# Performance work log

Hardware: AMD Instinct MI355X
Metric: run time of the kernel (lower is better)

## Reference

```python
import jax, jax.numpy as jnp
import numpy as np

R = 32  # voxel resolution


def setup_inputs() -> dict:
    key = jax.random.key(0)
    k1, k2 = jax.random.split(key)
    B, C, N = 8, 64, 100000
    features = jax.random.normal(k1, (B, C, N), dtype=jnp.float32)
    coords = jax.random.uniform(k2, (B, 3, N), dtype=jnp.float32)  # unit cube [0,1]
    return {"features": features, "coords": coords}


def reference(features, coords):
    # features: [B, C, N], coords: [B, 3, N] in [0, 1]
    B, C, N = features.shape
    norm_coords = jnp.clip(coords * R, 0, R - 1)
    vox_coords = jnp.round(norm_coords).astype(jnp.int32)  # [B, 3, N]

    # flat voxel index per point: x*R^2 + y*R + z, offset per batch
    idx = vox_coords[:, 0] * R * R + vox_coords[:, 1] * R + vox_coords[:, 2]  # [B, N]
    flat_idx = (idx + jnp.arange(B, dtype=jnp.int32)[:, None] * (R ** 3)).reshape(-1)  # [B*N]

    feat = jnp.transpose(features, (0, 2, 1)).reshape(B * N, C)  # [B*N, C]
    sums = jax.ops.segment_sum(feat, flat_idx, num_segments=B * R ** 3)  # [B*R^3, C]
    cnt = jax.ops.segment_sum(jnp.ones((B * N,), features.dtype), flat_idx,
                              num_segments=B * R ** 3)  # [B*R^3]
    avg = sums / jnp.maximum(cnt, 1.0)[:, None]  # average; empty voxels stay 0

    vox_feat = jnp.transpose(avg.reshape(B, R ** 3, C), (0, 2, 1)).reshape(B, C, R, R, R)
    return vox_feat, vox_coords.astype(jnp.int64)
```

## Files before the change

### kernel.cpp

```cpp
#include <hip/hip_runtime.h>

#define RR 32
#define R3 32768
#define BATCH 8
#define CH 64
#define NPTS 100000
#define NPOINTS (BATCH * NPTS)
#define NVOX (BATCH * R3)
#define SCAN_BLOCKS (NVOX / 256)
#define HBLK 32
#define PPB (NPTS / HBLK)

typedef unsigned int uint32;

__device__ __forceinline__ uint32 f2bf(float f) {
    uint32 u = __float_as_uint(f);
    return (u + 0x7fffu + ((u >> 16) & 1u)) >> 16;
}
__device__ __forceinline__ float bf2f(uint32 h) {
    return __uint_as_float(h << 16);
}

__global__ __launch_bounds__(256) void voxhist(
    const float* __restrict__ coords,
    uint32* __restrict__ vox,
    uint32* __restrict__ phist,
    float* __restrict__ out2)
{
    __shared__ uint32 hist[R3];

    int b   = blockIdx.x >> 5;
    int blk = blockIdx.x & 31;
    int tid = threadIdx.x;

    for (int i = tid; i < R3; i += 256) hist[i] = 0u;
    __syncthreads();

    int n0 = blk * PPB;
    const float* cb = coords + (size_t)b * 3 * NPTS;
    float*       o2 = out2   + (size_t)b * 3 * NPTS;

    for (int i = tid; i < PPB; i += 256) {
        int n = n0 + i;
        float fx = fminf(fmaxf(cb[n]            * 32.0f, 0.0f), 31.0f);
        float fy = fminf(fmaxf(cb[NPTS + n]     * 32.0f, 0.0f), 31.0f);
        float fz = fminf(fmaxf(cb[2 * NPTS + n] * 32.0f, 0.0f), 31.0f);
        int x = (int)rintf(fx);
        int y = (int)rintf(fy);
        int z = (int)rintf(fz);
        int v = x * (RR * RR) + y * RR + z;

        o2[n]            = (float)x;
        o2[NPTS + n]     = (float)y;
        o2[2 * NPTS + n] = (float)z;

        vox[(size_t)b * NPTS + n] = (uint32)(b * R3 + v);
        atomicAdd(&hist[v], 1u);
    }
    __syncthreads();

    uint32* ph = phist + (size_t)(b * HBLK + blk) * R3;
    for (int i = tid; i < R3; i += 256) ph[i] = hist[i];
}

__global__ __launch_bounds__(256) void scan_hist_sums(
    const uint32* __restrict__ phist,
    uint32* __restrict__ cnt, uint32* __restrict__ bsum)
{
    __shared__ uint32 s[256];
    int t = threadIdx.x;
    int gid = blockIdx.x * 256 + t;
    int b = gid >> 15;
    int v = gid & (R3 - 1);

    const uint32* ph = phist + (size_t)b * HBLK * R3 + v;
    uint32 c = 0;
#pragma unroll
    for (int k = 0; k < HBLK; ++k) c += ph[(size_t)k * R3];
    cnt[gid] = c;

    s[t] = c;
    __syncthreads();
    for (int off = 128; off > 0; off >>= 1) {
        if (t < off) s[t] += s[t + off];
        __syncthreads();
    }
    if (t == 0) bsum[blockIdx.x] = s[0];
}

__global__ __launch_bounds__(256) void scan_bsum(uint32* __restrict__ bsum)
{
    __shared__ uint32 s[256];
    int t = threadIdx.x;
    uint32 v0 = bsum[4 * t], v1 = bsum[4 * t + 1], v2 = bsum[4 * t + 2], v3 = bsum[4 * t + 3];
    uint32 tot = v0 + v1 + v2 + v3;
    s[t] = tot;
    __syncthreads();
    for (int off = 1; off < 256; off <<= 1) {
        uint32 x = (t >= off) ? s[t - off] : 0u;
        __syncthreads();
        s[t] += x;
        __syncthreads();
    }
    uint32 excl = s[t] - tot;
    bsum[4 * t]     = excl;
    bsum[4 * t + 1] = excl + v0;
    bsum[4 * t + 2] = excl + v0 + v1;
    bsum[4 * t + 3] = excl + v0 + v1 + v2;
}

__global__ __launch_bounds__(256) void scan_final(
    const uint32* __restrict__ cnt, const uint32* __restrict__ bsum,
    uint32* __restrict__ starts, uint32* __restrict__ cursor)
{
    __shared__ uint32 s[256];
    int t = threadIdx.x;
    int gid = blockIdx.x * 256 + t;
    uint32 v = cnt[gid];
    s[t] = v;
    __syncthreads();
    for (int off = 1; off < 256; off <<= 1) {
        uint32 x = (t >= off) ? s[t - off] : 0u;
        __syncthreads();
        s[t] += x;
        __syncthreads();
    }
    uint32 st = bsum[blockIdx.x] + s[t] - v;
    starts[gid] = st;
    cursor[gid] = st;
}

__global__ __launch_bounds__(256) void phase3_scatter(
    const float* __restrict__ feat,
    const uint32* __restrict__ vox,
    uint32* __restrict__ cursor,
    uint4* __restrict__ sorted)
{
    int gid = blockIdx.x * blockDim.x + threadIdx.x;
    if (gid >= NPOINTS) return;
    int b = gid / NPTS;
    int n = gid - b * NPTS;

    uint32 g = vox[gid];
    uint32 pos = atomicAdd(&cursor[g], 1u);

    const float* frow = feat + (size_t)b * CH * NPTS + n;
    uint4* dst = sorted + (size_t)pos * 8;
#pragma unroll
    for (int j = 0; j < 8; ++j) {
        uint4 w;
        float f0 = frow[(size_t)(8 * j + 0) * NPTS];
        float f1 = frow[(size_t)(8 * j + 1) * NPTS];
        float f2 = frow[(size_t)(8 * j + 2) * NPTS];
        float f3 = frow[(size_t)(8 * j + 3) * NPTS];
        float f4 = frow[(size_t)(8 * j + 4) * NPTS];
        float f5 = frow[(size_t)(8 * j + 5) * NPTS];
        float f6 = frow[(size_t)(8 * j + 6) * NPTS];
        float f7 = frow[(size_t)(8 * j + 7) * NPTS];
        w.x = f2bf(f0) | (f2bf(f1) << 16);
        w.y = f2bf(f2) | (f2bf(f3) << 16);
        w.z = f2bf(f4) | (f2bf(f5) << 16);
        w.w = f2bf(f6) | (f2bf(f7) << 16);
        dst[j] = w;
    }
}

__global__ __launch_bounds__(256) void phase4_reduce(
    const uint32* __restrict__ sorted,
    const uint32* __restrict__ starts,
    float* __restrict__ out1)
{
    __shared__ float tile[64][65];

    int gbase = blockIdx.x * 64;
    int tid = threadIdx.x;
    int w = tid >> 6, lane = tid & 63;
    int half = lane >> 5;
    int cp   = lane & 31;

    for (int k = 0; k < 16; ++k) {
        int g = gbase + w * 16 + k;
        uint32 s = starts[g];
        uint32 e = (g == NVOX - 1) ? (uint32)NPOINTS : starts[g + 1];
        float a0 = 0.0f, a1 = 0.0f;
        for (uint32 p = s + half; p < e; p += 2) {
            uint32 d = sorted[(size_t)p * 32 + cp];
            a0 += bf2f(d & 0xffffu);
            a1 += bf2f(d >> 16);
        }
        a0 += __shfl_xor(a0, 32);
        a1 += __shfl_xor(a1, 32);
        if (half == 0) {
            uint32 c = e - s;
            float rcp = 1.0f / (float)(c > 1u ? c : 1u);
            int vloc = w * 16 + k;
            tile[vloc][2 * cp]     = a0 * rcp;
            tile[vloc][2 * cp + 1] = a1 * rcp;
        }
    }
    __syncthreads();

    int b = gbase / R3;
    int v0 = gbase - b * R3;
    int vv = tid & 63;
    int c0 = tid >> 6;
    float* obase = out1 + (size_t)b * CH * R3 + v0 + vv;
#pragma unroll
    for (int jj = 0; jj < 16; ++jj) {
        int c = jj * 4 + c0;
        obase[(size_t)c * R3] = tile[vv][c];
    }
}

__global__ __launch_bounds__(256) void accum_direct(
    const float* __restrict__ feat, const float* __restrict__ coords,
    float* __restrict__ out1, uint32* __restrict__ cnt, float* __restrict__ out2)
{
    int gid = blockIdx.x * blockDim.x + threadIdx.x;
    if (gid >= NPOINTS) return;
    int b = gid / NPTS;
    int n = gid - b * NPTS;
    const float* cb = coords + (size_t)b * 3 * NPTS + n;
    float fx = fminf(fmaxf(cb[0]        * 32.0f, 0.0f), 31.0f);
    float fy = fminf(fmaxf(cb[NPTS]     * 32.0f, 0.0f), 31.0f);
    float fz = fminf(fmaxf(cb[2 * NPTS] * 32.0f, 0.0f), 31.0f);
    int x = (int)rintf(fx), y = (int)rintf(fy), z = (int)rintf(fz);
    int v = x * (RR * RR) + y * RR + z;
    float* o2 = out2 + (size_t)b * 3 * NPTS + n;
    o2[0] = (float)x; o2[NPTS] = (float)y; o2[2 * NPTS] = (float)z;
    atomicAdd(&cnt[b * R3 + v], 1u);
    float* obase = out1 + (size_t)(b * CH) * R3 + v;
    const float* frow = feat + (size_t)(b * CH) * NPTS + n;
#pragma unroll 8
    for (int c = 0; c < CH; ++c)
        unsafeAtomicAdd(&obase[(size_t)c * R3], frow[(size_t)c * NPTS]);
}

__global__ __launch_bounds__(256) void finalize_direct(
    float* __restrict__ out1, const uint32* __restrict__ cnt)
{
    size_t gid = (size_t)blockIdx.x * blockDim.x + threadIdx.x;
    size_t total = (size_t)BATCH * CH * R3;
    if (gid >= total) return;
    int v = (int)(gid & (R3 - 1));
    int b = (int)(gid / ((size_t)CH * R3));
    uint32 ct = cnt[b * R3 + v];
    out1[gid] = out1[gid] / (float)(ct > 1u ? ct : 1u);
}

extern "C" void kernel_launch(void* const* d_in, const int* in_sizes, int n_in,
                              void* d_out, int out_size, void* d_ws, size_t ws_size,
                              hipStream_t stream)
{
    const float* feat   = (const float*)d_in[0];
    const float* coords = (const float*)d_in[1];

    float* out1 = (float*)d_out;
    float* out2 = out1 + (size_t)BATCH * CH * R3;

    const size_t vox_off    = 0;
    const size_t vox_bytes  = (size_t)NPOINTS * 4;
    const size_t cnt_off    = vox_off + ((vox_bytes + 255) & ~255ull);
    const size_t cnt_bytes  = (size_t)NVOX * 4;
    const size_t starts_off = cnt_off + ((cnt_bytes + 255) & ~255ull);
    const size_t cursor_off = starts_off + ((cnt_bytes + 255) & ~255ull);
    const size_t bsum_off   = cursor_off + ((cnt_bytes + 255) & ~255ull);
    const size_t bsum_bytes = (size_t)SCAN_BLOCKS * 4;
    const size_t sort_off   = (bsum_off + bsum_bytes + 255) & ~255ull;
    const size_t sort_bytes = (size_t)NPOINTS * 128;
    const size_t need       = sort_off + sort_bytes;

    const int npt_blocks = (NPOINTS + 255) / 256;

    if (ws_size >= need) {
        char* ws = (char*)d_ws;
        uint32* vox    = (uint32*)(ws + vox_off);
        uint32* cnt    = (uint32*)(ws + cnt_off);
        uint32* starts = (uint32*)(ws + starts_off);
        uint32* cursor = (uint32*)(ws + cursor_off);
        uint32* bsum   = (uint32*)(ws + bsum_off);
        uint32* sorted = (uint32*)(ws + sort_off);
        uint32* phist  = sorted;

        voxhist<<<BATCH * HBLK, 256, 0, stream>>>(coords, vox, phist, out2);
        scan_hist_sums<<<SCAN_BLOCKS, 256, 0, stream>>>(phist, cnt, bsum);
        scan_bsum<<<1, 256, 0, stream>>>(bsum);
        scan_final<<<SCAN_BLOCKS, 256, 0, stream>>>(cnt, bsum, starts, cursor);
        phase3_scatter<<<npt_blocks, 256, 0, stream>>>(feat, vox, cursor, (uint4*)sorted);
        phase4_reduce<<<NVOX / 64, 256, 0, stream>>>(sorted, starts, out1);
    } else {
        uint32* cnt = (uint32*)d_ws;
        hipMemsetAsync(out1, 0, (size_t)BATCH * CH * R3 * sizeof(float), stream);
        hipMemsetAsync(d_ws, 0, (size_t)NVOX * 4, stream);
        accum_direct<<<npt_blocks, 256, 0, stream>>>(feat, coords, out1, cnt, out2);
        size_t total = (size_t)BATCH * CH * R3;
        finalize_direct<<<(unsigned)((total + 255) / 256), 256, 0, stream>>>(out1, cnt);
    }
}
```

Before: 445.0 us.

## Split scatter into coalesced bf16 transpose plus index-only counting sort and gather-reduce

Replaces the per-point scatter, which read 64 strided feature values and wrote a 128-byte bf16 row to a sorted position, with a shared-memory tiled transpose that writes point-major bf16 features coalesced. The scatter kernel now writes only a 4-byte point index, and the reduce kernel gathers feature rows through that index. Voxel indices are also stored as 16-bit values, and histogram clear and copy use 16-byte vector accesses. The aim is to replace strided, uncoalesced feature reads with coalesced ones, at the cost of an extra indirection and random row gathers in the reduce.

```diff
diff --git a/kernel.cpp b/kernel.cpp
--- a/kernel.cpp
+++ b/kernel.cpp
@@ -10,8 +10,10 @@
 #define SCAN_BLOCKS (NVOX / 256)
 #define HBLK 32
 #define PPB (NPTS / HBLK)
+#define NTILE 1563
 
 typedef unsigned int uint32;
+typedef unsigned short uint16;
 
 __device__ __forceinline__ uint32 f2bf(float f) {
     uint32 u = __float_as_uint(f);
@@ -23,7 +25,7 @@
 
 __global__ __launch_bounds__(256) void voxhist(
     const float* __restrict__ coords,
-    uint32* __restrict__ vox,
+    uint16* __restrict__ vox,
     uint32* __restrict__ phist,
     float* __restrict__ out2)
 {
@@ -33,7 +35,8 @@
     int blk = blockIdx.x & 31;
     int tid = threadIdx.x;
 
-    for (int i = tid; i < R3; i += 256) hist[i] = 0u;
+    uint4 z4 = make_uint4(0u, 0u, 0u, 0u);
+    for (int i = tid; i < R3 / 4; i += 256) ((uint4*)hist)[i] = z4;
     __syncthreads();
 
     int n0 = blk * PPB;
@@ -54,13 +57,13 @@
         o2[NPTS + n]     = (float)y;
         o2[2 * NPTS + n] = (float)z;
 
-        vox[(size_t)b * NPTS + n] = (uint32)(b * R3 + v);
+        vox[(size_t)b * NPTS + n] = (uint16)v;
         atomicAdd(&hist[v], 1u);
     }
     __syncthreads();
 
-    uint32* ph = phist + (size_t)(b * HBLK + blk) * R3;
-    for (int i = tid; i < R3; i += 256) ph[i] = hist[i];
+    uint4* ph = (uint4*)(phist + (size_t)(b * HBLK + blk) * R3);
+    for (int i = tid; i < R3 / 4; i += 256) ph[i] = ((const uint4*)hist)[i];
 }
 
 __global__ __launch_bounds__(256) void scan_hist_sums(
@@ -130,43 +133,63 @@
     cursor[gid] = st;
 }
 
-__global__ __launch_bounds__(256) void phase3_scatter(
+__global__ __launch_bounds__(256) void transpose_bf16(
     const float* __restrict__ feat,
-    const uint32* __restrict__ vox,
+    uint16* __restrict__ featT)
+{
+    __shared__ float tile[64][65];
+
+    int b    = blockIdx.x / NTILE;
+    int t    = blockIdx.x - b * NTILE;
+    int n0   = t * 64;
+    int tid  = threadIdx.x;
+
+    int i  = tid & 63;
+    int cq = tid >> 6;
+    const float* fb = feat + (size_t)b * CH * NPTS;
+    int n = n0 + i;
+    bool ok = (n < NPTS);
+#pragma unroll
+    for (int k = 0; k < 16; ++k) {
+        int c = cq * 16 + k;
+        float v = ok ? fb[(size_t)c * NPTS + n] : 0.0f;
+        tile[c][i] = v;
+    }
+    __syncthreads();
+
+    int q = tid & 7;
+#pragma unroll
+    for (int h = 0; h < 2; ++h) {
+        int r = (tid >> 3) + 32 * h;
+        int nr = n0 + r;
+        if (nr < NPTS) {
+            uint4 wv;
+            wv.x = f2bf(tile[8*q+0][r]) | (f2bf(tile[8*q+1][r]) << 16);
+            wv.y = f2bf(tile[8*q+2][r]) | (f2bf(tile[8*q+3][r]) << 16);
+            wv.z = f2bf(tile[8*q+4][r]) | (f2bf(tile[8*q+5][r]) << 16);
+            wv.w = f2bf(tile[8*q+6][r]) | (f2bf(tile[8*q+7][r]) << 16);
+            ((uint4*)featT)[((size_t)b * NPTS + nr) * 8 + q] = wv;
+        }
+    }
+}
+
+__global__ __launch_bounds__(256) void scatter_idx(
+    const uint16* __restrict__ vox,
     uint32* __restrict__ cursor,
-    uint4* __restrict__ sorted)
+    uint32* __restrict__ order)
 {
     int gid = blockIdx.x * blockDim.x + threadIdx.x;
     if (gid >= NPOINTS) return;
     int b = gid / NPTS;
     int n = gid - b * NPTS;
-
-    uint32 g = vox[gid];
+    uint32 g = (uint32)(b * R3 + (int)vox[gid]);
     uint32 pos = atomicAdd(&cursor[g], 1u);
-
-    const float* frow = feat + (size_t)b * CH * NPTS + n;
-    uint4* dst = sorted + (size_t)pos * 8;
-#pragma unroll
-    for (int j = 0; j < 8; ++j) {
-        uint4 w;
-        float f0 = frow[(size_t)(8 * j + 0) * NPTS];
-        float f1 = frow[(size_t)(8 * j + 1) * NPTS];
-        float f2 = frow[(size_t)(8 * j + 2) * NPTS];
-        float f3 = frow[(size_t)(8 * j + 3) * NPTS];
-        float f4 = frow[(size_t)(8 * j + 4) * NPTS];
-        float f5 = frow[(size_t)(8 * j + 5) * NPTS];
-        float f6 = frow[(size_t)(8 * j + 6) * NPTS];
-        float f7 = frow[(size_t)(8 * j + 7) * NPTS];
-        w.x = f2bf(f0) | (f2bf(f1) << 16);
-        w.y = f2bf(f2) | (f2bf(f3) << 16);
-        w.z = f2bf(f4) | (f2bf(f5) << 16);
-        w.w = f2bf(f6) | (f2bf(f7) << 16);
-        dst[j] = w;
-    }
-}
-
-__global__ __launch_bounds__(256) void phase4_reduce(
-    const uint32* __restrict__ sorted,
+    order[pos] = (uint32)n;
+}
+
+__global__ __launch_bounds__(256) void gather_reduce(
+    const uint32* __restrict__ order,
+    const uint32* __restrict__ featT,
     const uint32* __restrict__ starts,
     float* __restrict__ out1)
 {
@@ -177,6 +200,8 @@
     int w = tid >> 6, lane = tid & 63;
     int half = lane >> 5;
     int cp   = lane & 31;
+    int b = gbase >> 15;
+    const uint32* fTb = featT + (size_t)b * NPTS * 32;
 
     for (int k = 0; k < 16; ++k) {
         int g = gbase + w * 16 + k;
@@ -184,7 +209,8 @@
         uint32 e = (g == NVOX - 1) ? (uint32)NPOINTS : starts[g + 1];
         float a0 = 0.0f, a1 = 0.0f;
         for (uint32 p = s + half; p < e; p += 2) {
-            uint32 d = sorted[(size_t)p * 32 + cp];
+            uint32 n = order[p];
+            uint32 d = fTb[(size_t)n * 32 + cp];
             a0 += bf2f(d & 0xffffu);
             a1 += bf2f(d >> 16);
         }
@@ -200,7 +226,6 @@
     }
     __syncthreads();
 
-    int b = gbase / R3;
     int v0 = gbase - b * R3;
     int vv = tid & 63;
     int c0 = tid >> 6;
@@ -259,35 +284,40 @@
     float* out2 = out1 + (size_t)BATCH * CH * R3;
 
     const size_t vox_off    = 0;
-    const size_t vox_bytes  = (size_t)NPOINTS * 4;
+    const size_t vox_bytes  = (size_t)NPOINTS * 2;
     const size_t cnt_off    = vox_off + ((vox_bytes + 255) & ~255ull);
     const size_t cnt_bytes  = (size_t)NVOX * 4;
     const size_t starts_off = cnt_off + ((cnt_bytes + 255) & ~255ull);
     const size_t cursor_off = starts_off + ((cnt_bytes + 255) & ~255ull);
     const size_t bsum_off   = cursor_off + ((cnt_bytes + 255) & ~255ull);
     const size_t bsum_bytes = (size_t)SCAN_BLOCKS * 4;
-    const size_t sort_off   = (bsum_off + bsum_bytes + 255) & ~255ull;
-    const size_t sort_bytes = (size_t)NPOINTS * 128;
-    const size_t need       = sort_off + sort_bytes;
+    const size_t order_off  = (bsum_off + bsum_bytes + 255) & ~255ull;
+    const size_t order_bytes= (size_t)NPOINTS * 4;
+    const size_t featT_off  = (order_off + order_bytes + 255) & ~255ull;
+    const size_t featT_bytes= (size_t)NPOINTS * CH * 2;
+    const size_t need       = featT_off + featT_bytes;
 
     const int npt_blocks = (NPOINTS + 255) / 256;
 
     if (ws_size >= need) {
         char* ws = (char*)d_ws;
-        uint32* vox    = (uint32*)(ws + vox_off);
+        uint16* vox    = (uint16*)(ws + vox_off);
         uint32* cnt    = (uint32*)(ws + cnt_off);
         uint32* starts = (uint32*)(ws + starts_off);
         uint32* cursor = (uint32*)(ws + cursor_off);
         uint32* bsum   = (uint32*)(ws + bsum_off);
-        uint32* sorted = (uint32*)(ws + sort_off);
-        uint32* phist  = sorted;
+        uint32* order  = (uint32*)(ws + order_off);
+        uint16* featT  = (uint16*)(ws + featT_off);
+        uint32* phist  = (uint32*)featT;
 
         voxhist<<<BATCH * HBLK, 256, 0, stream>>>(coords, vox, phist, out2);
         scan_hist_sums<<<SCAN_BLOCKS, 256, 0, stream>>>(phist, cnt, bsum);
         scan_bsum<<<1, 256, 0, stream>>>(bsum);
         scan_final<<<SCAN_BLOCKS, 256, 0, stream>>>(cnt, bsum, starts, cursor);
-        phase3_scatter<<<npt_blocks, 256, 0, stream>>>(feat, vox, cursor, (uint4*)sorted);
-        phase4_reduce<<<NVOX / 64, 256, 0, stream>>>(sorted, starts, out1);
+        transpose_bf16<<<BATCH * NTILE, 256, 0, stream>>>(feat, featT);
+        scatter_idx<<<npt_blocks, 256, 0, stream>>>(vox, cursor, order);
+        gather_reduce<<<NVOX / 64, 256, 0, stream>>>(order, (const uint32*)featT,
+                                                     starts, out1);
     } else {
         uint32* cnt = (uint32*)d_ws;
         hipMemsetAsync(out1, 0, (size_t)BATCH * CH * R3 * sizeof(float), stream);
```

Result: slower. 467.8 us (+5.1%).

## Replace global cursor atomics with per-block histogram ranks for deterministic scatter

Applied to the files above, without the earlier changes.

The histogram kernel now records each point's local rank from the shared-memory atomicAdd, packed with its voxel id into the vox array. A new make_pbase kernel turns the per-block partial histograms into per-block base offsets, so the scatter kernel computes its destination without global atomics on a cursor array. The number of histogram blocks per batch drops from 32 to 8, which cuts histogram writeback and the summation over partials but leaves fewer blocks in the first kernel. A fallback path using global atomic counting is kept for smaller workspaces, and it needs a separate phist buffer, which raises the workspace requirement.

```diff
diff --git a/kernel.cpp b/kernel.cpp
--- a/kernel.cpp
+++ b/kernel.cpp
@@ -8,7 +8,7 @@
 #define NPOINTS (BATCH * NPTS)
 #define NVOX (BATCH * R3)
 #define SCAN_BLOCKS (NVOX / 256)
-#define HBLK 32
+#define HBLK 8
 #define PPB (NPTS / HBLK)
 
 typedef unsigned int uint32;
@@ -21,7 +21,7 @@
     return __uint_as_float(h << 16);
 }
 
-__global__ __launch_bounds__(256) void voxhist(
+__global__ __launch_bounds__(256) void voxrank(
     const float* __restrict__ coords,
     uint32* __restrict__ vox,
     uint32* __restrict__ phist,
@@ -29,11 +29,12 @@
 {
     __shared__ uint32 hist[R3];
 
-    int b   = blockIdx.x >> 5;
-    int blk = blockIdx.x & 31;
+    int b   = blockIdx.x >> 3;
+    int blk = blockIdx.x & 7;
     int tid = threadIdx.x;
 
-    for (int i = tid; i < R3; i += 256) hist[i] = 0u;
+    uint4 z4 = make_uint4(0u, 0u, 0u, 0u);
+    for (int i = tid; i < R3 / 4; i += 256) ((uint4*)hist)[i] = z4;
     __syncthreads();
 
     int n0 = blk * PPB;
@@ -54,13 +55,13 @@
         o2[NPTS + n]     = (float)y;
         o2[2 * NPTS + n] = (float)z;
 
-        vox[(size_t)b * NPTS + n] = (uint32)(b * R3 + v);
-        atomicAdd(&hist[v], 1u);
-    }
-    __syncthreads();
-
-    uint32* ph = phist + (size_t)(b * HBLK + blk) * R3;
-    for (int i = tid; i < R3; i += 256) ph[i] = hist[i];
+        uint32 r = atomicAdd(&hist[v], 1u);
+        vox[(size_t)b * NPTS + n] = (uint32)v | (r << 16);
+    }
+    __syncthreads();
+
+    uint4* ph = (uint4*)(phist + (size_t)(b * HBLK + blk) * R3);
+    for (int i = tid; i < R3 / 4; i += 256) ph[i] = ((const uint4*)hist)[i];
 }
 
 __global__ __launch_bounds__(256) void scan_hist_sums(
@@ -109,9 +110,9 @@
     bsum[4 * t + 3] = excl + v0 + v1 + v2;
 }
 
-__global__ __launch_bounds__(256) void scan_final(
+__global__ __launch_bounds__(256) void scan_starts(
     const uint32* __restrict__ cnt, const uint32* __restrict__ bsum,
-    uint32* __restrict__ starts, uint32* __restrict__ cursor)
+    uint32* __restrict__ starts)
 {
     __shared__ uint32 s[256];
     int t = threadIdx.x;
@@ -125,15 +126,30 @@
         s[t] += x;
         __syncthreads();
     }
-    uint32 st = bsum[blockIdx.x] + s[t] - v;
-    starts[gid] = st;
-    cursor[gid] = st;
-}
-
-__global__ __launch_bounds__(256) void phase3_scatter(
+    starts[gid] = bsum[blockIdx.x] + s[t] - v;
+}
+
+__global__ __launch_bounds__(256) void make_pbase(
+    uint32* __restrict__ phist,
+    const uint32* __restrict__ starts)
+{
+    int gid = blockIdx.x * 256 + threadIdx.x;
+    int b = gid >> 15;
+    int v = gid & (R3 - 1);
+    uint32 s = starts[gid];
+    uint32* ph = phist + (size_t)b * HBLK * R3 + v;
+#pragma unroll
+    for (int k = 0; k < HBLK; ++k) {
+        uint32 c = ph[(size_t)k * R3];
+        ph[(size_t)k * R3] = s;
+        s += c;
+    }
+}
+
+__global__ __launch_bounds__(256) void scatter_rank(
     const float* __restrict__ feat,
     const uint32* __restrict__ vox,
-    uint32* __restrict__ cursor,
+    const uint32* __restrict__ pbase,
     uint4* __restrict__ sorted)
 {
     int gid = blockIdx.x * blockDim.x + threadIdx.x;
@@ -141,8 +157,11 @@
     int b = gid / NPTS;
     int n = gid - b * NPTS;
 
-    uint32 g = vox[gid];
-    uint32 pos = atomicAdd(&cursor[g], 1u);
+    uint32 vr = vox[gid];
+    uint32 v  = vr & 0xffffu;
+    uint32 r  = vr >> 16;
+    int   blk = n / PPB;
+    uint32 pos = pbase[(size_t)(b * HBLK + blk) * R3 + v] + r;
 
     const float* frow = feat + (size_t)b * CH * NPTS + n;
     uint4* dst = sorted + (size_t)pos * 8;
@@ -212,6 +231,105 @@
     }
 }
 
+__global__ __launch_bounds__(256) void phase1_count(
+    const float* __restrict__ coords,
+    uint32* __restrict__ vox,
+    uint32* __restrict__ cnt,
+    float* __restrict__ out2)
+{
+    int gid = blockIdx.x * blockDim.x + threadIdx.x;
+    if (gid >= NPOINTS) return;
+    int b = gid / NPTS;
+    int n = gid - b * NPTS;
+
+    const float* cb = coords + (size_t)b * 3 * NPTS + n;
+    float fx = fminf(fmaxf(cb[0]        * 32.0f, 0.0f), 31.0f);
+    float fy = fminf(fmaxf(cb[NPTS]     * 32.0f, 0.0f), 31.0f);
+    float fz = fminf(fmaxf(cb[2 * NPTS] * 32.0f, 0.0f), 31.0f);
+    int x = (int)rintf(fx);
+    int y = (int)rintf(fy);
+    int z = (int)rintf(fz);
+    uint32 g = (uint32)(b * R3 + x * (RR * RR) + y * RR + z);
+
+    float* o2 = out2 + (size_t)b * 3 * NPTS + n;
+    o2[0]        = (float)x;
+    o2[NPTS]     = (float)y;
+    o2[2 * NPTS] = (float)z;
+
+    vox[gid] = g;
+    atomicAdd(&cnt[g], 1u);
+}
+
+__global__ __launch_bounds__(256) void scan_block_sums(
+    const uint32* __restrict__ cnt, uint32* __restrict__ bsum)
+{
+    __shared__ uint32 s[256];
+    int t = threadIdx.x;
+    s[t] = cnt[blockIdx.x * 256 + t];
+    __syncthreads();
+    for (int off = 128; off > 0; off >>= 1) {
+        if (t < off) s[t] += s[t + off];
+        __syncthreads();
+    }
+    if (t == 0) bsum[blockIdx.x] = s[0];
+}
+
+__global__ __launch_bounds__(256) void scan_final(
+    const uint32* __restrict__ cnt, const uint32* __restrict__ bsum,
+    uint32* __restrict__ starts, uint32* __restrict__ cursor)
+{
+    __shared__ uint32 s[256];
+    int t = threadIdx.x;
+    int gid = blockIdx.x * 256 + t;
+    uint32 v = cnt[gid];
+    s[t] = v;
+    __syncthreads();
+    for (int off = 1; off < 256; off <<= 1) {
+        uint32 x = (t >= off) ? s[t - off] : 0u;
+        __syncthreads();
+        s[t] += x;
+        __syncthreads();
+    }
+    uint32 st = bsum[blockIdx.x] + s[t] - v;
+    starts[gid] = st;
+    cursor[gid] = st;
+}
+
+__global__ __launch_bounds__(256) void phase3_scatter(
+    const float* __restrict__ feat,
+    const uint32* __restrict__ vox,
+    uint32* __restrict__ cursor,
+    uint4* __restrict__ sorted)
+{
+    int gid = blockIdx.x * blockDim.x + threadIdx.x;
+    if (gid >= NPOINTS) return;
+    int b = gid / NPTS;
+    int n = gid - b * NPTS;
+
+    uint32 g = vox[gid];
+    uint32 pos = atomicAdd(&cursor[g], 1u);
+
+    const float* frow = feat + (size_t)b * CH * NPTS + n;
+    uint4* dst = sorted + (size_t)pos * 8;
+#pragma unroll
+    for (int j = 0; j < 8; ++j) {
+        uint4 w;
+        float f0 = frow[(size_t)(8 * j + 0) * NPTS];
+        float f1 = frow[(size_t)(8 * j + 1) * NPTS];
+        float f2 = frow[(size_t)(8 * j + 2) * NPTS];
+        float f3 = frow[(size_t)(8 * j + 3) * NPTS];
+        float f4 = frow[(size_t)(8 * j + 4) * NPTS];
+        float f5 = frow[(size_t)(8 * j + 5) * NPTS];
+        float f6 = frow[(size_t)(8 * j + 6) * NPTS];
+        float f7 = frow[(size_t)(8 * j + 7) * NPTS];
+        w.x = f2bf(f0) | (f2bf(f1) << 16);
+        w.y = f2bf(f2) | (f2bf(f3) << 16);
+        w.z = f2bf(f4) | (f2bf(f5) << 16);
+        w.w = f2bf(f6) | (f2bf(f7) << 16);
+        dst[j] = w;
+    }
+}
+
 __global__ __launch_bounds__(256) void accum_direct(
     const float* __restrict__ feat, const float* __restrict__ coords,
     float* __restrict__ out1, uint32* __restrict__ cnt, float* __restrict__ out2)
@@ -263,27 +381,49 @@
     const size_t cnt_off    = vox_off + ((vox_bytes + 255) & ~255ull);
     const size_t cnt_bytes  = (size_t)NVOX * 4;
     const size_t starts_off = cnt_off + ((cnt_bytes + 255) & ~255ull);
-    const size_t cursor_off = starts_off + ((cnt_bytes + 255) & ~255ull);
-    const size_t bsum_off   = cursor_off + ((cnt_bytes + 255) & ~255ull);
+    const size_t bsum_off   = starts_off + ((cnt_bytes + 255) & ~255ull);
     const size_t bsum_bytes = (size_t)SCAN_BLOCKS * 4;
-    const size_t sort_off   = (bsum_off + bsum_bytes + 255) & ~255ull;
+    const size_t phist_off  = (bsum_off + bsum_bytes + 255) & ~255ull;
+    const size_t phist_bytes= (size_t)BATCH * HBLK * R3 * 4;
+    const size_t sortA_off  = (phist_off + phist_bytes + 255) & ~255ull;
     const size_t sort_bytes = (size_t)NPOINTS * 128;
-    const size_t need       = sort_off + sort_bytes;
+    const size_t need_rank  = sortA_off + sort_bytes;
+
+    const size_t cursor_off = bsum_off;
+    const size_t bsumB_off  = cursor_off + ((cnt_bytes + 255) & ~255ull);
+    const size_t sortB_off  = (bsumB_off + bsum_bytes + 255) & ~255ull;
+    const size_t need_cur   = sortB_off + sort_bytes;
 
     const int npt_blocks = (NPOINTS + 255) / 256;
 
-    if (ws_size >= need) {
+    if (ws_size >= need_rank) {
+        char* ws = (char*)d_ws;
+        uint32* vox    = (uint32*)(ws + vox_off);
+        uint32* cnt    = (uint32*)(ws + cnt_off);
+        uint32* starts = (uint32*)(ws + starts_off);
+        uint32* bsum   = (uint32*)(ws + bsum_off);
+        uint32* phist  = (uint32*)(ws + phist_off);
+        uint32* sorted = (uint32*)(ws + sortA_off);
+
+        voxrank<<<BATCH * HBLK, 256, 0, stream>>>(coords, vox, phist, out2);
+        scan_hist_sums<<<SCAN_BLOCKS, 256, 0, stream>>>(phist, cnt, bsum);
+        scan_bsum<<<1, 256, 0, stream>>>(bsum);
+        scan_starts<<<SCAN_BLOCKS, 256, 0, stream>>>(cnt, bsum, starts);
+        make_pbase<<<SCAN_BLOCKS, 256, 0, stream>>>(phist, starts);
+        scatter_rank<<<npt_blocks, 256, 0, stream>>>(feat, vox, phist, (uint4*)sorted);
+        phase4_reduce<<<NVOX / 64, 256, 0, stream>>>(sorted, starts, out1);
+    } else if (ws_size >= need_cur) {
         char* ws = (char*)d_ws;
         uint32* vox    = (uint32*)(ws + vox_off);
         uint32* cnt    = (uint32*)(ws + cnt_off);
         uint32* starts = (uint32*)(ws + starts_off);
         uint32* cursor = (uint32*)(ws + cursor_off);
-        uint32* bsum   = (uint32*)(ws + bsum_off);
-        uint32* sorted = (uint32*)(ws + sort_off);
-        uint32* phist  = sorted;
-
-        voxhist<<<BATCH * HBLK, 256, 0, stream>>>(coords, vox, phist, out2);
-        scan_hist_sums<<<SCAN_BLOCKS, 256, 0, stream>>>(phist, cnt, bsum);
+        uint32* bsum   = (uint32*)(ws + bsumB_off);
+        uint32* sorted = (uint32*)(ws + sortB_off);
+
+        hipMemsetAsync(cnt, 0, cnt_bytes, stream);
+        phase1_count<<<npt_blocks, 256, 0, stream>>>(coords, vox, cnt, out2);
+        scan_block_sums<<<SCAN_BLOCKS, 256, 0, stream>>>(cnt, bsum);
         scan_bsum<<<1, 256, 0, stream>>>(bsum);
         scan_final<<<SCAN_BLOCKS, 256, 0, stream>>>(cnt, bsum, starts, cursor);
         phase3_scatter<<<npt_blocks, 256, 0, stream>>>(feat, vox, cursor, (uint4*)sorted);
```

New measurement: 479.2 us. 1.08x slower.
